# Performance work log

Measured on AMD Instinct MI355X. Metric: run time of the kernel, lower is better.

## Reference

```python
import jax, jax.numpy as jnp
import numpy as np

TOP_K = 2


def setup_inputs() -> dict:
    key = jax.random.key(0)
    ks = jax.random.split(key, 5)
    B, S, D, F, E = 2, 1024, 2048, 4096, 8
    scale_in = 1.0 / np.sqrt(D)
    scale_f = 1.0 / np.sqrt(F)
    return {
        "hidden_states": jax.random.normal(ks[0], (B, S, D), dtype=jnp.float32),
        "gate_w": jax.random.normal(ks[1], (D, E), dtype=jnp.float32) * scale_in,
        "w1": jax.random.normal(ks[2], (E, D, F), dtype=jnp.float32) * scale_in,
        "w3": jax.random.normal(ks[3], (E, D, F), dtype=jnp.float32) * scale_in,
        "w2": jax.random.normal(ks[4], (E, F, D), dtype=jnp.float32) * scale_f,
    }


def reference(hidden_states, gate_w, w1, w3, w2):
    orig_shape = hidden_states.shape
    D = orig_shape[-1]
    x = hidden_states.reshape(-1, D)                      # [T, D]
    E = gate_w.shape[-1]

    # Router: replicated linear (no bias), logits in fp32.
    router_logits = (x @ gate_w).astype(jnp.float32)      # [T, E]
    probs = jax.nn.softmax(router_logits, axis=-1)        # [T, E]
    topk_vals, topk_idx = jax.lax.top_k(probs, TOP_K)     # [T, K]
    # renormalize=False: use raw softmax probs of the selected experts.
    # Scatter top-k weights back to a dense [T, E] combine matrix.
    onehot = jax.nn.one_hot(topk_idx, E, dtype=probs.dtype)        # [T, K, E]
    combine = jnp.einsum("tke,tk->te", onehot, topk_vals)          # [T, E]

    # Dense-over-experts SwiGLU (reference for the fused grouped-GEMM).
    gate = jax.nn.silu(jnp.einsum("td,edf->etf", x, w1))  # [E, T, F]
    up = jnp.einsum("td,edf->etf", x, w3)                 # [E, T, F]
    expert_out = jnp.einsum("etf,efd->etd", gate * up, w2)  # [E, T, D]

    # Combine (this is the TP all-reduce + weighted sum in vllm).
    y = jnp.einsum("te,etd->td", combine, expert_out)     # [T, D]
    return y.reshape(orig_shape)
```

## Files before the change

### kernel.cpp

```cpp
#include <hip/hip_runtime.h>

typedef short v8s __attribute__((ext_vector_type(8)));
typedef float v4f __attribute__((ext_vector_type(4)));
typedef float v16f __attribute__((ext_vector_type(16)));

#define T_TOK 2048
#define DD 2048
#define FF 4096
#define EE 8
#define BM 128
#define BN 128
#define BK 64
#define MT_MAX 40
#define MAXROWS 5120

#define WS_COUNTS 0
#define WS_FILL   32
#define WS_ROWOFF 64
#define WS_TOPE   128
#define WS_TOPW   (WS_TOPE + T_TOK * 2 * 4)
#define WS_IDS    (WS_TOPW + T_TOK * 2 * 4)
#define WS_WTS    (WS_IDS + MAXROWS * 4)
#define WS_ZERO   (WS_WTS + MAXROWS * 4)
#define WS_XB     73984ul
#define WS_H      (WS_XB + 8388608ul)

#define SWZ(r, kb) ((r) * 128 + ((kb) ^ ((((r) ^ ((r) >> 3)) & 7) << 4)))

static __device__ __forceinline__ short f2bf(float f) {
  return __builtin_bit_cast(short, static_cast<__bf16>(f));
}

__global__ __launch_bounds__(256) void xbf_k(const float* __restrict__ x,
                                             unsigned short* __restrict__ xb) {
  const int i = (blockIdx.x * 256 + threadIdx.x) * 8;
  v4f a = *(const v4f*)(x + i);
  v4f b = *(const v4f*)(x + i + 4);
  v8s h;
  h[0] = f2bf(a[0]); h[1] = f2bf(a[1]); h[2] = f2bf(a[2]); h[3] = f2bf(a[3]);
  h[4] = f2bf(b[0]); h[5] = f2bf(b[1]); h[6] = f2bf(b[2]); h[7] = f2bf(b[3]);
  *(v8s*)(xb + i) = h;
}

__global__ __launch_bounds__(256) void router_k(
    const float* __restrict__ x, const float* __restrict__ gw,
    int* __restrict__ counts, int* __restrict__ tope, float* __restrict__ topw) {
  const int lane = threadIdx.x & 63;
  const int t = blockIdx.x * 4 + (threadIdx.x >> 6);
  if (t >= T_TOK) return;
  float acc[EE] = {0.f, 0.f, 0.f, 0.f, 0.f, 0.f, 0.f, 0.f};
  const float* xr = x + (size_t)t * DD;
  for (int i = 0; i < DD / 64; ++i) {
    int k = i * 64 + lane;
    float xv = xr[k];
    const v4f* g = (const v4f*)(gw + (size_t)k * EE);
    v4f g0 = g[0], g1 = g[1];
    acc[0] += xv * g0[0]; acc[1] += xv * g0[1]; acc[2] += xv * g0[2]; acc[3] += xv * g0[3];
    acc[4] += xv * g1[0]; acc[5] += xv * g1[1]; acc[6] += xv * g1[2]; acc[7] += xv * g1[3];
  }
  #pragma unroll
  for (int e = 0; e < EE; ++e) {
    #pragma unroll
    for (int off = 32; off > 0; off >>= 1) acc[e] += __shfl_xor(acc[e], off);
  }
  if (lane == 0) {
    float m = acc[0];
    #pragma unroll
    for (int e = 1; e < EE; ++e) m = fmaxf(m, acc[e]);
    float p[EE], s = 0.f;
    #pragma unroll
    for (int e = 0; e < EE; ++e) { p[e] = expf(acc[e] - m); s += p[e]; }
    float inv = 1.f / s;
    #pragma unroll
    for (int e = 0; e < EE; ++e) p[e] *= inv;
    int e1 = 0;
    #pragma unroll
    for (int e = 1; e < EE; ++e) if (p[e] > p[e1]) e1 = e;
    int e2 = (e1 == 0) ? 1 : 0;
    #pragma unroll
    for (int e = 0; e < EE; ++e) if (e != e1 && p[e] > p[e2]) e2 = e;
    tope[2 * t] = e1;  tope[2 * t + 1] = e2;
    topw[2 * t] = p[e1]; topw[2 * t + 1] = p[e2];
    atomicAdd(&counts[e1], 1);
    atomicAdd(&counts[e2], 1);
  }
}

__global__ void offsets_k(const int* __restrict__ counts, int* __restrict__ rowoff) {
  if (threadIdx.x == 0) {
    int off = 0;
    #pragma unroll
    for (int e = 0; e < EE; ++e) {
      rowoff[e] = off;
      off += ((counts[e] + BM - 1) / BM) * BM;
    }
  }
}

__global__ __launch_bounds__(256) void scatter_k(
    const int* __restrict__ tope, const float* __restrict__ topw,
    const int* __restrict__ rowoff, int* __restrict__ fill,
    int* __restrict__ ids, float* __restrict__ wts) {
  const int t = blockIdx.x * 256 + threadIdx.x;
  if (t >= T_TOK) return;
  #pragma unroll
  for (int j = 0; j < 2; ++j) {
    int e = tope[2 * t + j];
    int pos = rowoff[e] + atomicAdd(&fill[e], 1);
    ids[pos] = t;
    wts[pos] = topw[2 * t + j];
  }
}

static __device__ __forceinline__ int find_expert(
    const int* counts, const int* rowoff, int mt) {
  int expert = -1;
  #pragma unroll
  for (int e = 0; e < EE; ++e) {
    int rs = rowoff[e];
    int tl = (counts[e] + BM - 1) / BM;
    if (mt * BM >= rs && mt * BM < rs + tl * BM) expert = e;
  }
  return expert;
}

static __device__ __forceinline__ void xcd_map(int* nt, int* mt) {
  int gx = gridDim.x, gy = gridDim.y;
  int nwg = gx * gy;
  int lin = blockIdx.y * gx + blockIdx.x;
  int q = nwg >> 3;
  int s = (lin & 7) * q + (lin >> 3);
  *nt = s / gy;
  *mt = s % gy;
}

__global__ __launch_bounds__(256, 2) void gemm1_k(
    const unsigned short* __restrict__ xb, const float* __restrict__ w1,
    const float* __restrict__ w3, const int* __restrict__ counts,
    const int* __restrict__ rowoff, const int* __restrict__ ids,
    unsigned short* __restrict__ H) {
  int nt, mt;
  xcd_map(&nt, &mt);
  const int expert = find_expert(counts, rowoff, mt);
  if (expert < 0) return;
  const int m0 = mt * BM, n0 = nt * BN;

  __shared__ unsigned short sA[BM * BK];
  __shared__ unsigned short sB0[BN * BK];
  __shared__ unsigned short sB1[BN * BK];

  const int tid = threadIdx.x;
  const int lane = tid & 63;
  const int wid = tid >> 6;
  const int wm = (wid >> 1) * 64, wn = (wid & 1) * 64;
  const int l32 = lane & 31;
  const int khi = lane >> 5;

  const int a_row0 = tid >> 3;
  const int a_ch = tid & 7;
  const unsigned short* aptr[4];
  #pragma unroll
  for (int g = 0; g < 4; ++g)
    aptr[g] = xb + (size_t)ids[m0 + a_row0 + g * 32] * DD + a_ch * 8;

  const int b_f4 = (tid & 31) * 4;
  const int b_k8 = (tid >> 5) * 8;
  const float* wb1 = w1 + (size_t)expert * DD * FF + n0 + b_f4 + (size_t)b_k8 * FF;
  const float* wb3 = w3 + (size_t)expert * DD * FF + n0 + b_f4 + (size_t)b_k8 * FF;

  v16f acc1[2][2], acc3[2][2];
  #pragma unroll
  for (int i = 0; i < 2; ++i)
    #pragma unroll
    for (int j = 0; j < 2; ++j) {
      acc1[i][j] = (v16f)(0.f);
      acc3[i][j] = (v16f)(0.f);
    }

  for (int kt = 0; kt < DD / BK; ++kt) {
    #pragma unroll
    for (int g = 0; g < 4; ++g) {
      v8s h = *(const v8s*)(aptr[g] + (size_t)kt * BK);
      *(v8s*)((char*)sA + SWZ(a_row0 + g * 32, a_ch * 16)) = h;
    }
    {
      const float* p = wb1 + (size_t)kt * BK * FF;
      v4f r[8];
      #pragma unroll
      for (int j = 0; j < 8; ++j) r[j] = *(const v4f*)(p + (size_t)j * FF);
      #pragma unroll
      for (int c = 0; c < 4; ++c) {
        v8s h;
        #pragma unroll
        for (int j = 0; j < 8; ++j) h[j] = f2bf(r[j][c]);
        *(v8s*)((char*)sB0 + SWZ(b_f4 + c, b_k8 * 2)) = h;
      }
      p = wb3 + (size_t)kt * BK * FF;
      #pragma unroll
      for (int j = 0; j < 8; ++j) r[j] = *(const v4f*)(p + (size_t)j * FF);
      #pragma unroll
      for (int c = 0; c < 4; ++c) {
        v8s h;
        #pragma unroll
        for (int j = 0; j < 8; ++j) h[j] = f2bf(r[j][c]);
        *(v8s*)((char*)sB1 + SWZ(b_f4 + c, b_k8 * 2)) = h;
      }
    }
    __syncthreads();
    #pragma unroll
    for (int ks = 0; ks < 4; ++ks) {
      const int kb = (ks * 2 + khi) * 16;
      v8s a[2], b1[2], b3[2];
      #pragma unroll
      for (int m = 0; m < 2; ++m)
        a[m] = *(const v8s*)((const char*)sA + SWZ(wm + m * 32 + l32, kb));
      #pragma unroll
      for (int n = 0; n < 2; ++n) {
        b1[n] = *(const v8s*)((const char*)sB0 + SWZ(wn + n * 32 + l32, kb));
        b3[n] = *(const v8s*)((const char*)sB1 + SWZ(wn + n * 32 + l32, kb));
      }
      #pragma unroll
      for (int m = 0; m < 2; ++m)
        #pragma unroll
        for (int n = 0; n < 2; ++n) {
          acc1[m][n] = __builtin_amdgcn_mfma_f32_32x32x16_bf16(a[m], b1[n], acc1[m][n], 0, 0, 0);
          acc3[m][n] = __builtin_amdgcn_mfma_f32_32x32x16_bf16(a[m], b3[n], acc3[m][n], 0, 0, 0);
        }
    }
    __syncthreads();
  }
  #pragma unroll
  for (int m = 0; m < 2; ++m)
    #pragma unroll
    for (int n = 0; n < 2; ++n)
      #pragma unroll
      for (int r = 0; r < 16; ++r) {
        int row = wm + m * 32 + (r & 3) + 8 * (r >> 2) + 4 * khi;
        int col = wn + n * 32 + l32;
        float g = acc1[m][n][r];
        float u = acc3[m][n][r];
        float hv = (g / (1.f + expf(-g))) * u;
        H[(size_t)(m0 + row) * FF + (n0 + col)] = (unsigned short)f2bf(hv);
      }
}

__global__ __launch_bounds__(256, 2) void gemm2_k(
    const unsigned short* __restrict__ H, const float* __restrict__ w2,
    const int* __restrict__ counts, const int* __restrict__ rowoff,
    const int* __restrict__ ids, const float* __restrict__ wts,
    float* __restrict__ out) {
  int nt, mt;
  xcd_map(&nt, &mt);
  const int expert = find_expert(counts, rowoff, mt);
  if (expert < 0) return;
  const int m0 = mt * BM, n0 = nt * BN;

  __shared__ unsigned short sA[BM * BK];
  __shared__ unsigned short sB[BN * BK];

  const int tid = threadIdx.x;
  const int lane = tid & 63;
  const int wid = tid >> 6;
  const int wm = (wid >> 1) * 64, wn = (wid & 1) * 64;
  const int l32 = lane & 31;
  const int khi = lane >> 5;

  const int a_row0 = tid >> 3;
  const int a_ch = tid & 7;
  const unsigned short* ha = H + (size_t)(m0 + a_row0) * FF + a_ch * 8;
  const int b_f4 = (tid & 31) * 4;
  const int b_k8 = (tid >> 5) * 8;
  const float* wb = w2 + (size_t)expert * FF * DD + n0 + b_f4 + (size_t)b_k8 * DD;

  v16f acc[2][2];
  #pragma unroll
  for (int i = 0; i < 2; ++i)
    #pragma unroll
    for (int j = 0; j < 2; ++j) acc[i][j] = (v16f)(0.f);

  for (int kt = 0; kt < FF / BK; ++kt) {
    #pragma unroll
    for (int g = 0; g < 4; ++g) {
      v8s h = *(const v8s*)(ha + (size_t)g * 32 * FF + kt * BK);
      *(v8s*)((char*)sA + SWZ(a_row0 + g * 32, a_ch * 16)) = h;
    }
    {
      const float* p = wb + (size_t)kt * BK * DD;
      v4f r[8];
      #pragma unroll
      for (int j = 0; j < 8; ++j) r[j] = *(const v4f*)(p + (size_t)j * DD);
      #pragma unroll
      for (int c = 0; c < 4; ++c) {
        v8s h;
        #pragma unroll
        for (int j = 0; j < 8; ++j) h[j] = f2bf(r[j][c]);
        *(v8s*)((char*)sB + SWZ(b_f4 + c, b_k8 * 2)) = h;
      }
    }
    __syncthreads();
    #pragma unroll
    for (int ks = 0; ks < 4; ++ks) {
      const int kb = (ks * 2 + khi) * 16;
      v8s a[2], b[2];
      #pragma unroll
      for (int m = 0; m < 2; ++m)
        a[m] = *(const v8s*)((const char*)sA + SWZ(wm + m * 32 + l32, kb));
      #pragma unroll
      for (int n = 0; n < 2; ++n)
        b[n] = *(const v8s*)((const char*)sB + SWZ(wn + n * 32 + l32, kb));
      #pragma unroll
      for (int m = 0; m < 2; ++m)
        #pragma unroll
        for (int n = 0; n < 2; ++n)
          acc[m][n] = __builtin_amdgcn_mfma_f32_32x32x16_bf16(a[m], b[n], acc[m][n], 0, 0, 0);
    }
    __syncthreads();
  }
  #pragma unroll
  for (int m = 0; m < 2; ++m)
    #pragma unroll
    for (int r = 0; r < 16; ++r) {
      int row = m0 + wm + m * 32 + (r & 3) + 8 * (r >> 2) + 4 * khi;
      float wgt = wts[row];
      if (wgt != 0.f) {
        float* orow = out + (size_t)ids[row] * DD + n0 + wn + l32;
        #pragma unroll
        for (int n = 0; n < 2; ++n)
          atomicAdd(orow + n * 32, wgt * acc[m][n][r]);
      }
    }
}

extern "C" void kernel_launch(void* const* d_in, const int* in_sizes, int n_in,
                              void* d_out, int out_size, void* d_ws, size_t ws_size,
                              hipStream_t stream) {
  const float* x  = (const float*)d_in[0];
  const float* gw = (const float*)d_in[1];
  const float* w1 = (const float*)d_in[2];
  const float* w3 = (const float*)d_in[3];
  const float* w2 = (const float*)d_in[4];
  float* out = (float*)d_out;
  char* ws = (char*)d_ws;

  int*   counts = (int*)(ws + WS_COUNTS);
  int*   fill   = (int*)(ws + WS_FILL);
  int*   rowoff = (int*)(ws + WS_ROWOFF);
  int*   tope   = (int*)(ws + WS_TOPE);
  float* topw   = (float*)(ws + WS_TOPW);
  int*   ids    = (int*)(ws + WS_IDS);
  float* wts    = (float*)(ws + WS_WTS);
  unsigned short* xb = (unsigned short*)(ws + WS_XB);
  unsigned short* H  = (unsigned short*)(ws + WS_H);

  hipMemsetAsync(ws, 0, WS_ZERO, stream);
  hipMemsetAsync(d_out, 0, (size_t)out_size * sizeof(float), stream);

  xbf_k<<<T_TOK * DD / (256 * 8), 256, 0, stream>>>(x, xb);
  router_k<<<T_TOK / 4, 256, 0, stream>>>(x, gw, counts, tope, topw);
  offsets_k<<<1, 64, 0, stream>>>(counts, rowoff);
  scatter_k<<<T_TOK / 256, 256, 0, stream>>>(tope, topw, rowoff, fill, ids, wts);
  gemm1_k<<<dim3(FF / BN, MT_MAX), 256, 0, stream>>>(xb, w1, w3, counts, rowoff, ids, H);
  gemm2_k<<<dim3(DD / BN, MT_MAX), 256, 0, stream>>>(H, w2, counts, rowoff, ids, wts, out);
}
```

Baseline: 545.0 us.

## Prefetch weight tiles into registers and load activations directly to LDS

Both grouped GEMM kernels now load the bf16 activation tile with global_load_lds, writing straight into LDS with a pre-swizzled source address, and skip the register round-trip. The fp32 weight tile for the next K step is prefetched into registers while the current step computes. Explicit vmcnt/lgkmcnt waits, raw barriers and sched_barriers replace __syncthreads. This should hide global load latency behind MFMA work. The cost is more live registers and reliance on hand-counted wait counts for correctness.

```diff
diff --git a/kernel.cpp b/kernel.cpp
--- a/kernel.cpp
+++ b/kernel.cpp
@@ -25,10 +25,23 @@
 #define WS_XB     73984ul
 #define WS_H      (WS_XB + 8388608ul)
 
-#define SWZ(r, kb) ((r) * 128 + ((kb) ^ ((((r) ^ ((r) >> 3)) & 7) << 4)))
+#define SW(r)     ((((r) ^ ((r) >> 3)) & 7))
+#define SWZ(r, kb) ((r) * 128 + ((kb) ^ (SW(r) << 4)))
+
+#define VMCNTN(N) asm volatile("s_waitcnt vmcnt(" #N ")" ::: "memory")
+#define VMCNT0()  asm volatile("s_waitcnt vmcnt(0)" ::: "memory")
+#define LGKM0()   asm volatile("s_waitcnt lgkmcnt(0)" ::: "memory")
+#define BARR()    __builtin_amdgcn_s_barrier()
+#define SCHEDB()  __builtin_amdgcn_sched_barrier(0)
 
 static __device__ __forceinline__ short f2bf(float f) {
   return __builtin_bit_cast(short, static_cast<__bf16>(f));
+}
+
+static __device__ __forceinline__ void gload_lds16(const void* g, void* l) {
+  __builtin_amdgcn_global_load_lds(
+      (const __attribute__((address_space(1))) unsigned int*)g,
+      (__attribute__((address_space(3))) unsigned int*)l, 16, 0, 0);
 }
 
 __global__ __launch_bounds__(256) void xbf_k(const float* __restrict__ x,
@@ -156,18 +169,36 @@
   const int l32 = lane & 31;
   const int khi = lane >> 5;
 
-  const int a_row0 = tid >> 3;
-  const int a_ch = tid & 7;
-  const unsigned short* aptr[4];
-  #pragma unroll
-  for (int g = 0; g < 4; ++g)
-    aptr[g] = xb + (size_t)ids[m0 + a_row0 + g * 32] * DD + a_ch * 8;
+  const unsigned short* ga[4];
+  #pragma unroll
+  for (int i = 0; i < 4; ++i) {
+    int r = wid * 32 + i * 8 + (lane >> 3);
+    ga[i] = xb + (size_t)ids[m0 + r] * DD + (((lane & 7) ^ SW(r)) << 3);
+  }
 
   const int b_f4 = (tid & 31) * 4;
   const int b_k8 = (tid >> 5) * 8;
   const float* wb1 = w1 + (size_t)expert * DD * FF + n0 + b_f4 + (size_t)b_k8 * FF;
   const float* wb3 = w3 + (size_t)expert * DD * FF + n0 + b_f4 + (size_t)b_k8 * FF;
 
+  v4f r1[8], r3[8];
+  #define G1_ALDS(KT) { _Pragma("unroll") for (int i_ = 0; i_ < 4; ++i_)        \
+      gload_lds16(ga[i_] + (size_t)(KT) * BK,                                   \
+                  (char*)sA + (wid * 32 + i_ * 8) * 128); }
+  #define G1_BL(KT) {                                                           \
+      const float* p_ = wb1 + (size_t)(KT) * BK * FF;                           \
+      _Pragma("unroll") for (int j_ = 0; j_ < 8; ++j_)                          \
+        r1[j_] = *(const v4f*)(p_ + (size_t)j_ * FF);                           \
+      p_ = wb3 + (size_t)(KT) * BK * FF;                                        \
+      _Pragma("unroll") for (int j_ = 0; j_ < 8; ++j_)                          \
+        r3[j_] = *(const v4f*)(p_ + (size_t)j_ * FF); }
+  #define G1_BW() { _Pragma("unroll") for (int c_ = 0; c_ < 4; ++c_) {          \
+      v8s h1_, h3_;                                                             \
+      _Pragma("unroll") for (int j_ = 0; j_ < 8; ++j_) {                        \
+        h1_[j_] = f2bf(r1[j_][c_]); h3_[j_] = f2bf(r3[j_][c_]); }               \
+      *(v8s*)((char*)sB0 + SWZ(b_f4 + c_, b_k8 * 2)) = h1_;                     \
+      *(v8s*)((char*)sB1 + SWZ(b_f4 + c_, b_k8 * 2)) = h3_; } }
+
   v16f acc1[2][2], acc3[2][2];
   #pragma unroll
   for (int i = 0; i < 2; ++i)
@@ -177,36 +208,21 @@
       acc3[i][j] = (v16f)(0.f);
     }
 
+  G1_BL(0);
+
   for (int kt = 0; kt < DD / BK; ++kt) {
-    #pragma unroll
-    for (int g = 0; g < 4; ++g) {
-      v8s h = *(const v8s*)(aptr[g] + (size_t)kt * BK);
-      *(v8s*)((char*)sA + SWZ(a_row0 + g * 32, a_ch * 16)) = h;
-    }
-    {
-      const float* p = wb1 + (size_t)kt * BK * FF;
-      v4f r[8];
-      #pragma unroll
-      for (int j = 0; j < 8; ++j) r[j] = *(const v4f*)(p + (size_t)j * FF);
-      #pragma unroll
-      for (int c = 0; c < 4; ++c) {
-        v8s h;
-        #pragma unroll
-        for (int j = 0; j < 8; ++j) h[j] = f2bf(r[j][c]);
-        *(v8s*)((char*)sB0 + SWZ(b_f4 + c, b_k8 * 2)) = h;
-      }
-      p = wb3 + (size_t)kt * BK * FF;
-      #pragma unroll
-      for (int j = 0; j < 8; ++j) r[j] = *(const v4f*)(p + (size_t)j * FF);
-      #pragma unroll
-      for (int c = 0; c < 4; ++c) {
-        v8s h;
-        #pragma unroll
-        for (int j = 0; j < 8; ++j) h[j] = f2bf(r[j][c]);
-        *(v8s*)((char*)sB1 + SWZ(b_f4 + c, b_k8 * 2)) = h;
-      }
-    }
-    __syncthreads();
+    G1_ALDS(kt);
+    SCHEDB();
+    G1_BW();
+    if (kt + 1 < DD / BK) {
+      G1_BL(kt + 1);
+      SCHEDB();
+      VMCNTN(16);
+    } else {
+      VMCNT0();
+    }
+    LGKM0(); BARR();
+    SCHEDB();
     #pragma unroll
     for (int ks = 0; ks < 4; ++ks) {
       const int kb = (ks * 2 + khi) * 16;
@@ -227,7 +243,7 @@
           acc3[m][n] = __builtin_amdgcn_mfma_f32_32x32x16_bf16(a[m], b3[n], acc3[m][n], 0, 0, 0);
         }
     }
-    __syncthreads();
+    BARR();
   }
   #pragma unroll
   for (int m = 0; m < 2; ++m)
@@ -265,39 +281,50 @@
   const int l32 = lane & 31;
   const int khi = lane >> 5;
 
-  const int a_row0 = tid >> 3;
-  const int a_ch = tid & 7;
-  const unsigned short* ha = H + (size_t)(m0 + a_row0) * FF + a_ch * 8;
+  const unsigned short* ga[4];
+  #pragma unroll
+  for (int i = 0; i < 4; ++i) {
+    int r = wid * 32 + i * 8 + (lane >> 3);
+    ga[i] = H + (size_t)(m0 + r) * FF + (((lane & 7) ^ SW(r)) << 3);
+  }
+
   const int b_f4 = (tid & 31) * 4;
   const int b_k8 = (tid >> 5) * 8;
   const float* wb = w2 + (size_t)expert * FF * DD + n0 + b_f4 + (size_t)b_k8 * DD;
 
+  v4f rb[8];
+  #define G2_ALDS(KT) { _Pragma("unroll") for (int i_ = 0; i_ < 4; ++i_)        \
+      gload_lds16(ga[i_] + (size_t)(KT) * BK,                                   \
+                  (char*)sA + (wid * 32 + i_ * 8) * 128); }
+  #define G2_BL(KT) { const float* p_ = wb + (size_t)(KT) * BK * DD;            \
+      _Pragma("unroll") for (int j_ = 0; j_ < 8; ++j_)                          \
+        rb[j_] = *(const v4f*)(p_ + (size_t)j_ * DD); }
+  #define G2_BW() { _Pragma("unroll") for (int c_ = 0; c_ < 4; ++c_) {          \
+      v8s h_;                                                                   \
+      _Pragma("unroll") for (int j_ = 0; j_ < 8; ++j_) h_[j_] = f2bf(rb[j_][c_]);\
+      *(v8s*)((char*)sB + SWZ(b_f4 + c_, b_k8 * 2)) = h_; } }
+
   v16f acc[2][2];
   #pragma unroll
   for (int i = 0; i < 2; ++i)
     #pragma unroll
     for (int j = 0; j < 2; ++j) acc[i][j] = (v16f)(0.f);
 
+  G2_BL(0);
+
   for (int kt = 0; kt < FF / BK; ++kt) {
-    #pragma unroll
-    for (int g = 0; g < 4; ++g) {
-      v8s h = *(const v8s*)(ha + (size_t)g * 32 * FF + kt * BK);
-      *(v8s*)((char*)sA + SWZ(a_row0 + g * 32, a_ch * 16)) = h;
-    }
-    {
-      const float* p = wb + (size_t)kt * BK * DD;
-      v4f r[8];
-      #pragma unroll
-      for (int j = 0; j < 8; ++j) r[j] = *(const v4f*)(p + (size_t)j * DD);
-      #pragma unroll
-      for (int c = 0; c < 4; ++c) {
-        v8s h;
-        #pragma unroll
-        for (int j = 0; j < 8; ++j) h[j] = f2bf(r[j][c]);
-        *(v8s*)((char*)sB + SWZ(b_f4 + c, b_k8 * 2)) = h;
-      }
-    }
-    __syncthreads();
+    G2_ALDS(kt);
+    SCHEDB();
+    G2_BW();
+    if (kt + 1 < FF / BK) {
+      G2_BL(kt + 1);
+      SCHEDB();
+      VMCNTN(8);
+    } else {
+      VMCNT0();
+    }
+    LGKM0(); BARR();
+    SCHEDB();
     #pragma unroll
     for (int ks = 0; ks < 4; ++ks) {
       const int kb = (ks * 2 + khi) * 16;
@@ -314,7 +341,7 @@
         for (int n = 0; n < 2; ++n)
           acc[m][n] = __builtin_amdgcn_mfma_f32_32x32x16_bf16(a[m], b[n], acc[m][n], 0, 0, 0);
     }
-    __syncthreads();
+    BARR();
   }
   #pragma unroll
   for (int m = 0; m < 2; ++m)
```

New measurement: 514.2 us. 5.6% less time.
